# Optimization experiments

Measured on AMD Instinct MI355X. Metric: run time of the kernel, lower is better.

Reference implementation:

```python
import jax, jax.numpy as jnp
import numpy as np

N_ENVS, N_AGENTS, OBS_DIM, HIDDEN, HEAD = 4096, 64, 256, 512, 32


def setup_inputs() -> dict:
    key = jax.random.key(0)
    ks = jax.random.split(key, 10)
    s = 0.02
    return {
        "obs": jax.random.normal(ks[0], (N_ENVS, N_AGENTS, OBS_DIM), jnp.float32),
        # shared 2-layer MLP params (applied identically to every agent slice)
        "W1": jax.random.normal(ks[1], (OBS_DIM, HIDDEN), jnp.float32) * s,
        "b1": jnp.zeros((HIDDEN,), jnp.float32),
        "W2": jax.random.normal(ks[2], (HIDDEN, HIDDEN), jnp.float32) * s,
        "b2": jnp.zeros((HIDDEN,), jnp.float32),
        # per-agent head params, stacked over agent axis
        "HW1": jax.random.normal(ks[3], (N_AGENTS, HIDDEN, HEAD), jnp.float32) * s,
        "Hb1": jnp.zeros((N_AGENTS, HEAD), jnp.float32),
        "HW2": jax.random.normal(ks[4], (N_AGENTS, HEAD), jnp.float32) * s,
        "Hb2": jnp.zeros((N_AGENTS,), jnp.float32),
    }


def reference(obs, W1, b1, W2, b2, HW1, Hb1, HW2, Hb2):
    # shared MLP: same weights for every agent -> single batched GEMM over (env, agent)
    h = jax.nn.relu(jnp.einsum('ead,dh->eah', obs, W1) + b1)   # [E, A, H]
    feat = jax.nn.relu(jnp.einsum('eah,hk->eak', h, W2) + b2)  # [E, A, H]
    # per-agent heads: grouped GEMM via einsum over stacked weights
    g = jax.nn.relu(jnp.einsum('eah,ahk->eak', feat, HW1) + Hb1)  # [E, A, 32]
    actions = jax.nn.sigmoid(jnp.einsum('eak,ak->ea', g, HW2) + Hb2)  # [E, A]
    return actions
```

## Files before the change

kernel.cpp:

```cpp
#include <hip/hip_runtime.h>
#include <hip/hip_bf16.h>
#include <math.h>

#define N_ENVS   4096
#define N_AGENTS 64
#define OBS_DIM  256
#define HIDDEN   512
#define HEADK    32
#define BROWS    128

typedef __attribute__((ext_vector_type(8))) short bf16x8;
typedef __attribute__((ext_vector_type(4))) float f32x4;

static __device__ __forceinline__ unsigned cvt_pk_bf16(float lo, float hi) {
    unsigned r;
    asm("v_cvt_pk_bf16_f32 %0, %1, %2" : "=v"(r) : "v"(lo), "v"(hi));
    return r;
}

static __device__ __forceinline__ unsigned short f2bf(float x) {
    union { float f; unsigned int u; } v; v.f = x;
    unsigned int r = (v.u + 0x7FFFu + ((v.u >> 16) & 1u)) >> 16;
    return (unsigned short)r;
}

__global__ void prep_weights_kernel(const float* __restrict__ W1,
                                    const float* __restrict__ W2,
                                    const float* __restrict__ HW1,
                                    unsigned short* __restrict__ W1T,
                                    unsigned short* __restrict__ W2T,
                                    unsigned short* __restrict__ HW1T) {
    int id = blockIdx.x * 256 + threadIdx.x;
    if (id < 131072) {
        int k = id >> 9, n = id & 511;
        W1T[n * 256 + k] = f2bf(W1[id]);
    } else if (id < 131072 + 262144) {
        int t = id - 131072;
        int k = t >> 9, n = t & 511;
        W2T[n * 512 + k] = f2bf(W2[t]);
    } else if (id < 131072 + 262144 + 1048576) {
        int t = id - (131072 + 262144);
        int ag = t >> 14;
        int rem = t & 16383;
        int hh = rem >> 5, c = rem & 31;
        HW1T[((ag << 5) + c) * 512 + hh] = f2bf(HW1[t]);
    }
}

__launch_bounds__(512, 2)
__global__ void fused_mlp_kernel(const float* __restrict__ obs,
                                 const float* __restrict__ b1,
                                 const float* __restrict__ b2,
                                 const float* __restrict__ Hb1,
                                 const float* __restrict__ HW2,
                                 const float* __restrict__ Hb2,
                                 const unsigned short* __restrict__ W1T,
                                 const unsigned short* __restrict__ W2T,
                                 const unsigned short* __restrict__ HW1T,
                                 float* __restrict__ out) {
    __shared__ unsigned short buf[BROWS * 512];
    __shared__ float gpart[BROWS * 36];

    const int tid  = threadIdx.x;
    const int lane = tid & 63;
    const int wid  = tid >> 6;
    const int l15  = lane & 15;
    const int lk   = lane >> 4;
    const int e0   = blockIdx.x * 64;
    const int ap   = blockIdx.y;

    const f32x4 fzero = {0.f, 0.f, 0.f, 0.f};

    const unsigned short* bbase1 = W1T + (size_t)(wid * 64 + l15) * 256 + lk * 8;
    const unsigned short* bbase2 = W2T + (size_t)(wid * 64 + l15) * 512 + lk * 8;

    bf16x8 bcur[4];

    {
        const float* base = obs + (size_t)(((unsigned)e0 * 64u + 2u * (unsigned)ap) * 256u);
        float4 v[16];
        #pragma unroll
        for (int g = 0; g < 8; ++g) {
            unsigned gi  = (unsigned)tid + 512u * g;
            unsigned row = gi >> 5;
            unsigned kg  = (gi & 31u) << 3;
            unsigned fidx = (row & 63u) * 16384u + (row >> 6) * 256u + kg;
            v[2 * g]     = *reinterpret_cast<const float4*>(base + fidx);
            v[2 * g + 1] = *reinterpret_cast<const float4*>(base + fidx + 4);
        }
        #pragma unroll
        for (int ni = 0; ni < 4; ++ni)
            bcur[ni] = *reinterpret_cast<const bf16x8*>(bbase1 + ni * 16 * 256);
        #pragma unroll
        for (int g = 0; g < 8; ++g) {
            unsigned gi  = (unsigned)tid + 512u * g;
            unsigned row = gi >> 5;
            unsigned kg  = (gi & 31u) << 3;
            uint4 w;
            w.x = cvt_pk_bf16(v[2 * g].x, v[2 * g].y);
            w.y = cvt_pk_bf16(v[2 * g].z, v[2 * g].w);
            w.z = cvt_pk_bf16(v[2 * g + 1].x, v[2 * g + 1].y);
            w.w = cvt_pk_bf16(v[2 * g + 1].z, v[2 * g + 1].w);
            unsigned byt = (row * 512u + kg * 2u) ^ ((row & 7u) << 4);
            *reinterpret_cast<uint4*>(&buf[byt >> 1]) = w;
        }
    }
    __syncthreads();

    f32x4 acc[8][4];
    #pragma unroll
    for (int i = 0; i < 8; ++i)
        #pragma unroll
        for (int j = 0; j < 4; ++j) acc[i][j] = fzero;

    {
        #pragma unroll 1
        for (int ks = 0; ks < 8; ++ks) {
            bf16x8 bnxt[4];
            const int kn = (ks < 7 ? ks + 1 : 7);
            #pragma unroll
            for (int ni = 0; ni < 4; ++ni)
                bnxt[ni] = *reinterpret_cast<const bf16x8*>(bbase1 + ni * 16 * 256 + kn * 32);
            const int kk = ks * 32 + lk * 8;
            #pragma unroll
            for (int mi = 0; mi < 8; ++mi) {
                int row = mi * 16 + l15;
                bf16x8 af = *reinterpret_cast<const bf16x8*>(&buf[((row * 512 + kk * 2) ^ ((row & 7) << 4)) >> 1]);
                #pragma unroll
                for (int ni = 0; ni < 4; ++ni)
                    acc[mi][ni] = __builtin_amdgcn_mfma_f32_16x16x32_bf16(bcur[ni], af, acc[mi][ni], 0, 0, 0);
            }
            #pragma unroll
            for (int ni = 0; ni < 4; ++ni) bcur[ni] = bnxt[ni];
        }
    }

    bf16x8 bcur2[4];
    #pragma unroll
    for (int ni = 0; ni < 4; ++ni)
        bcur2[ni] = *reinterpret_cast<const bf16x8*>(bbase2 + ni * 16 * 512);

    __syncthreads();

    #pragma unroll
    for (int ni = 0; ni < 4; ++ni) {
        const int col0 = wid * 64 + ni * 16 + lk * 4;
        const float4 bias = *reinterpret_cast<const float4*>(b1 + col0);
        #pragma unroll
        for (int mi = 0; mi < 8; ++mi) {
            int row = mi * 16 + l15;
            float v0 = fmaxf(acc[mi][ni][0] + bias.x, 0.f);
            float v1 = fmaxf(acc[mi][ni][1] + bias.y, 0.f);
            float v2 = fmaxf(acc[mi][ni][2] + bias.z, 0.f);
            float v3 = fmaxf(acc[mi][ni][3] + bias.w, 0.f);
            uint2 w = { cvt_pk_bf16(v0, v1), cvt_pk_bf16(v2, v3) };
            int byt = (row * 1024 + col0 * 2) ^ ((row & 7) << 4);
            *reinterpret_cast<uint2*>(&buf[byt >> 1]) = w;
        }
    }
    __syncthreads();

    #pragma unroll
    for (int i = 0; i < 8; ++i)
        #pragma unroll
        for (int j = 0; j < 4; ++j) acc[i][j] = fzero;

    {
        #pragma unroll 1
        for (int ks = 0; ks < 16; ++ks) {
            bf16x8 bnxt[4];
            const int kn = (ks < 15 ? ks + 1 : 15);
            #pragma unroll
            for (int ni = 0; ni < 4; ++ni)
                bnxt[ni] = *reinterpret_cast<const bf16x8*>(bbase2 + ni * 16 * 512 + kn * 32);
            const int kk = ks * 32 + lk * 8;
            #pragma unroll
            for (int mi = 0; mi < 8; ++mi) {
                int row = mi * 16 + l15;
                bf16x8 af = *reinterpret_cast<const bf16x8*>(&buf[((row * 1024 + kk * 2) ^ ((row & 7) << 4)) >> 1]);
                #pragma unroll
                for (int ni = 0; ni < 4; ++ni)
                    acc[mi][ni] = __builtin_amdgcn_mfma_f32_16x16x32_bf16(bcur2[ni], af, acc[mi][ni], 0, 0, 0);
            }
            #pragma unroll
            for (int ni = 0; ni < 4; ++ni) bcur2[ni] = bnxt[ni];
        }
    }
    __syncthreads();

    #pragma unroll
    for (int ni = 0; ni < 4; ++ni) {
        const int col0 = wid * 64 + ni * 16 + lk * 4;
        const float4 bias = *reinterpret_cast<const float4*>(b2 + col0);
        #pragma unroll
        for (int mi = 0; mi < 8; ++mi) {
            int row = mi * 16 + l15;
            float v0 = fmaxf(acc[mi][ni][0] + bias.x, 0.f);
            float v1 = fmaxf(acc[mi][ni][1] + bias.y, 0.f);
            float v2 = fmaxf(acc[mi][ni][2] + bias.z, 0.f);
            float v3 = fmaxf(acc[mi][ni][3] + bias.w, 0.f);
            uint2 w = { cvt_pk_bf16(v0, v1), cvt_pk_bf16(v2, v3) };
            int byt = (row * 1024 + col0 * 2) ^ ((row & 7) << 4);
            *reinterpret_cast<uint2*>(&buf[byt >> 1]) = w;
        }
    }
    __syncthreads();

    {
        const int ja  = wid >> 2;
        const int hm  = wid & 3;
        const int a32 = ((2 * ap + ja) << 5);
        const unsigned short* hbase = HW1T + (size_t)(a32 + l15) * 512 + lk * 8;
        const int rowh = ja * 64 + hm * 16 + l15;
        f32x4 hacc[2] = {fzero, fzero};

        {
            bf16x8 hw0[8], hw1[8];
            #pragma unroll
            for (int ks = 0; ks < 8; ++ks) {
                hw0[ks] = *reinterpret_cast<const bf16x8*>(hbase + ks * 32);
                hw1[ks] = *reinterpret_cast<const bf16x8*>(hbase + 16 * 512 + ks * 32);
            }
            #pragma unroll
            for (int ks = 0; ks < 8; ++ks) {
                const int kk = ks * 32 + lk * 8;
                int byt = (rowh * 1024 + kk * 2) ^ ((rowh & 7) << 4);
                bf16x8 afh = *reinterpret_cast<const bf16x8*>(&buf[byt >> 1]);
                hacc[0] = __builtin_amdgcn_mfma_f32_16x16x32_bf16(hw0[ks], afh, hacc[0], 0, 0, 0);
                hacc[1] = __builtin_amdgcn_mfma_f32_16x16x32_bf16(hw1[ks], afh, hacc[1], 0, 0, 0);
            }
        }
        {
            bf16x8 hw0[8], hw1[8];
            #pragma unroll
            for (int ks = 0; ks < 8; ++ks) {
                hw0[ks] = *reinterpret_cast<const bf16x8*>(hbase + (ks + 8) * 32);
                hw1[ks] = *reinterpret_cast<const bf16x8*>(hbase + 16 * 512 + (ks + 8) * 32);
            }
            #pragma unroll
            for (int ks = 0; ks < 8; ++ks) {
                const int kk = (ks + 8) * 32 + lk * 8;
                int byt = (rowh * 1024 + kk * 2) ^ ((rowh & 7) << 4);
                bf16x8 afh = *reinterpret_cast<const bf16x8*>(&buf[byt >> 1]);
                hacc[0] = __builtin_amdgcn_mfma_f32_16x16x32_bf16(hw0[ks], afh, hacc[0], 0, 0, 0);
                hacc[1] = __builtin_amdgcn_mfma_f32_16x16x32_bf16(hw1[ks], afh, hacc[1], 0, 0, 0);
            }
        }

        #pragma unroll
        for (int ni = 0; ni < 2; ++ni) {
            const int col0 = ni * 16 + lk * 4;
            const float4 hbias = *reinterpret_cast<const float4*>(Hb1 + a32 + col0);
            float4 g;
            g.x = fmaxf(hacc[ni][0] + hbias.x, 0.f);
            g.y = fmaxf(hacc[ni][1] + hbias.y, 0.f);
            g.z = fmaxf(hacc[ni][2] + hbias.z, 0.f);
            g.w = fmaxf(hacc[ni][3] + hbias.w, 0.f);
            *reinterpret_cast<float4*>(&gpart[rowh * 36 + col0]) = g;
        }
    }
    __syncthreads();

    if (tid < BROWS) {
        int e = tid & 63, j = tid >> 6;
        int a = 2 * ap + j;
        float x = Hb2[a];
        #pragma unroll 2
        for (int k = 0; k < 32; ++k)
            x += gpart[tid * 36 + k] * HW2[(a << 5) + k];
        out[(size_t)(e0 + e) * N_AGENTS + a] = 1.f / (1.f + expf(-x));
    }
}

extern "C" void kernel_launch(void* const* d_in, const int* in_sizes, int n_in,
                              void* d_out, int out_size, void* d_ws, size_t ws_size,
                              hipStream_t stream) {
    const float* obs = (const float*)d_in[0];
    const float* W1  = (const float*)d_in[1];
    const float* b1  = (const float*)d_in[2];
    const float* W2  = (const float*)d_in[3];
    const float* b2  = (const float*)d_in[4];
    const float* HW1 = (const float*)d_in[5];
    const float* Hb1 = (const float*)d_in[6];
    const float* HW2 = (const float*)d_in[7];
    const float* Hb2 = (const float*)d_in[8];
    float* out = (float*)d_out;

    unsigned short* W1T  = (unsigned short*)d_ws;
    unsigned short* W2T  = W1T + 131072;
    unsigned short* HW1T = W2T + 262144;

    prep_weights_kernel<<<5632, 256, 0, stream>>>(W1, W2, HW1, W1T, W2T, HW1T);

    dim3 grid(N_ENVS / 64, N_AGENTS / 2);
    fused_mlp_kernel<<<grid, 512, 0, stream>>>(obs, b1, b2, Hb1, HW2, Hb2,
                                               W1T, W2T, HW1T, out);
}
```

Baseline: 325.9 us.

## Make fused MLP kernel persistent over eight env tiles with prefetched obs loads

The grid shrinks from 2048 blocks to 256 persistent blocks. Each block loops over 8 consecutive 64-env tiles for one agent pair. The obs loads for the next tile are issued before the head GEMM of the current tile, and are converted and stored to LDS after it, so global latency overlaps compute. The head weight loads become a software-pipelined loop instead of fully preloading 16 registers per half. The risk is fewer blocks than one per CU on a 256-CU device, with no block-level latency hiding, plus higher register pressure from holding the prefetched obs values.

```diff
diff --git a/kernel.cpp b/kernel.cpp
--- a/kernel.cpp
+++ b/kernel.cpp
@@ -66,31 +66,32 @@
     const int wid  = tid >> 6;
     const int l15  = lane & 15;
     const int lk   = lane >> 4;
-    const int e0   = blockIdx.x * 64;
-    const int ap   = blockIdx.y;
+    const int ap   = blockIdx.x & 31;
+    const int oct  = blockIdx.x >> 5;
 
     const f32x4 fzero = {0.f, 0.f, 0.f, 0.f};
 
     const unsigned short* bbase1 = W1T + (size_t)(wid * 64 + l15) * 256 + lk * 8;
     const unsigned short* bbase2 = W2T + (size_t)(wid * 64 + l15) * 512 + lk * 8;
 
-    bf16x8 bcur[4];
-
+    unsigned g_fidx[8];
+    #pragma unroll
+    for (int g = 0; g < 8; ++g) {
+        unsigned gi  = (unsigned)tid + 512u * g;
+        unsigned row = gi >> 5;
+        unsigned kg  = (gi & 31u) << 3;
+        g_fidx[g] = (row & 63u) * 16384u + (row >> 6) * 256u + kg;
+    }
+    const unsigned tile0_base = ((unsigned)(oct * 512) * 64u + 2u * (unsigned)ap) * 256u;
+
+    float4 v[16];
     {
-        const float* base = obs + (size_t)(((unsigned)e0 * 64u + 2u * (unsigned)ap) * 256u);
-        float4 v[16];
+        const float* base = obs + tile0_base;
         #pragma unroll
         for (int g = 0; g < 8; ++g) {
-            unsigned gi  = (unsigned)tid + 512u * g;
-            unsigned row = gi >> 5;
-            unsigned kg  = (gi & 31u) << 3;
-            unsigned fidx = (row & 63u) * 16384u + (row >> 6) * 256u + kg;
-            v[2 * g]     = *reinterpret_cast<const float4*>(base + fidx);
-            v[2 * g + 1] = *reinterpret_cast<const float4*>(base + fidx + 4);
-        }
-        #pragma unroll
-        for (int ni = 0; ni < 4; ++ni)
-            bcur[ni] = *reinterpret_cast<const bf16x8*>(bbase1 + ni * 16 * 256);
+            v[2 * g]     = *reinterpret_cast<const float4*>(base + g_fidx[g]);
+            v[2 * g + 1] = *reinterpret_cast<const float4*>(base + g_fidx[g] + 4);
+        }
         #pragma unroll
         for (int g = 0; g < 8; ++g) {
             unsigned gi  = (unsigned)tid + 512u * g;
@@ -105,170 +106,183 @@
             *reinterpret_cast<uint4*>(&buf[byt >> 1]) = w;
         }
     }
-    __syncthreads();
-
-    f32x4 acc[8][4];
-    #pragma unroll
-    for (int i = 0; i < 8; ++i)
-        #pragma unroll
-        for (int j = 0; j < 4; ++j) acc[i][j] = fzero;
-
-    {
-        #pragma unroll 1
-        for (int ks = 0; ks < 8; ++ks) {
-            bf16x8 bnxt[4];
-            const int kn = (ks < 7 ? ks + 1 : 7);
+
+    #pragma unroll 1
+    for (int t = 0; t < 8; ++t) {
+        __syncthreads();
+
+        f32x4 acc[8][4];
+        #pragma unroll
+        for (int i = 0; i < 8; ++i)
+            #pragma unroll
+            for (int j = 0; j < 4; ++j) acc[i][j] = fzero;
+
+        {
+            bf16x8 bcur[4];
             #pragma unroll
             for (int ni = 0; ni < 4; ++ni)
-                bnxt[ni] = *reinterpret_cast<const bf16x8*>(bbase1 + ni * 16 * 256 + kn * 32);
-            const int kk = ks * 32 + lk * 8;
+                bcur[ni] = *reinterpret_cast<const bf16x8*>(bbase1 + ni * 16 * 256);
+            #pragma unroll 1
+            for (int ks = 0; ks < 8; ++ks) {
+                bf16x8 bnxt[4];
+                const int kn = (ks < 7 ? ks + 1 : 7);
+                #pragma unroll
+                for (int ni = 0; ni < 4; ++ni)
+                    bnxt[ni] = *reinterpret_cast<const bf16x8*>(bbase1 + ni * 16 * 256 + kn * 32);
+                const int kk = ks * 32 + lk * 8;
+                #pragma unroll
+                for (int mi = 0; mi < 8; ++mi) {
+                    int row = mi * 16 + l15;
+                    bf16x8 af = *reinterpret_cast<const bf16x8*>(&buf[((row * 512 + kk * 2) ^ ((row & 7) << 4)) >> 1]);
+                    #pragma unroll
+                    for (int ni = 0; ni < 4; ++ni)
+                        acc[mi][ni] = __builtin_amdgcn_mfma_f32_16x16x32_bf16(bcur[ni], af, acc[mi][ni], 0, 0, 0);
+                }
+                #pragma unroll
+                for (int ni = 0; ni < 4; ++ni) bcur[ni] = bnxt[ni];
+            }
+        }
+
+        bf16x8 bcur2[4];
+        #pragma unroll
+        for (int ni = 0; ni < 4; ++ni)
+            bcur2[ni] = *reinterpret_cast<const bf16x8*>(bbase2 + ni * 16 * 512);
+
+        __syncthreads();
+
+        #pragma unroll
+        for (int ni = 0; ni < 4; ++ni) {
+            const int col0 = wid * 64 + ni * 16 + lk * 4;
+            const float4 bias = *reinterpret_cast<const float4*>(b1 + col0);
             #pragma unroll
             for (int mi = 0; mi < 8; ++mi) {
                 int row = mi * 16 + l15;
-                bf16x8 af = *reinterpret_cast<const bf16x8*>(&buf[((row * 512 + kk * 2) ^ ((row & 7) << 4)) >> 1]);
+                float v0 = fmaxf(acc[mi][ni][0] + bias.x, 0.f);
+                float v1 = fmaxf(acc[mi][ni][1] + bias.y, 0.f);
+                float v2 = fmaxf(acc[mi][ni][2] + bias.z, 0.f);
+                float v3 = fmaxf(acc[mi][ni][3] + bias.w, 0.f);
+                uint2 w = { cvt_pk_bf16(v0, v1), cvt_pk_bf16(v2, v3) };
+                int byt = (row * 1024 + col0 * 2) ^ ((row & 7) << 4);
+                *reinterpret_cast<uint2*>(&buf[byt >> 1]) = w;
+            }
+        }
+        __syncthreads();
+
+        #pragma unroll
+        for (int i = 0; i < 8; ++i)
+            #pragma unroll
+            for (int j = 0; j < 4; ++j) acc[i][j] = fzero;
+
+        {
+            #pragma unroll 1
+            for (int ks = 0; ks < 16; ++ks) {
+                bf16x8 bnxt[4];
+                const int kn = (ks < 15 ? ks + 1 : 15);
                 #pragma unroll
                 for (int ni = 0; ni < 4; ++ni)
-                    acc[mi][ni] = __builtin_amdgcn_mfma_f32_16x16x32_bf16(bcur[ni], af, acc[mi][ni], 0, 0, 0);
-            }
-            #pragma unroll
-            for (int ni = 0; ni < 4; ++ni) bcur[ni] = bnxt[ni];
-        }
-    }
-
-    bf16x8 bcur2[4];
-    #pragma unroll
-    for (int ni = 0; ni < 4; ++ni)
-        bcur2[ni] = *reinterpret_cast<const bf16x8*>(bbase2 + ni * 16 * 512);
-
-    __syncthreads();
-
-    #pragma unroll
-    for (int ni = 0; ni < 4; ++ni) {
-        const int col0 = wid * 64 + ni * 16 + lk * 4;
-        const float4 bias = *reinterpret_cast<const float4*>(b1 + col0);
-        #pragma unroll
-        for (int mi = 0; mi < 8; ++mi) {
-            int row = mi * 16 + l15;
-            float v0 = fmaxf(acc[mi][ni][0] + bias.x, 0.f);
-            float v1 = fmaxf(acc[mi][ni][1] + bias.y, 0.f);
-            float v2 = fmaxf(acc[mi][ni][2] + bias.z, 0.f);
-            float v3 = fmaxf(acc[mi][ni][3] + bias.w, 0.f);
-            uint2 w = { cvt_pk_bf16(v0, v1), cvt_pk_bf16(v2, v3) };
-            int byt = (row * 1024 + col0 * 2) ^ ((row & 7) << 4);
-            *reinterpret_cast<uint2*>(&buf[byt >> 1]) = w;
-        }
-    }
-    __syncthreads();
-
-    #pragma unroll
-    for (int i = 0; i < 8; ++i)
-        #pragma unroll
-        for (int j = 0; j < 4; ++j) acc[i][j] = fzero;
-
-    {
-        #pragma unroll 1
-        for (int ks = 0; ks < 16; ++ks) {
-            bf16x8 bnxt[4];
-            const int kn = (ks < 15 ? ks + 1 : 15);
-            #pragma unroll
-            for (int ni = 0; ni < 4; ++ni)
-                bnxt[ni] = *reinterpret_cast<const bf16x8*>(bbase2 + ni * 16 * 512 + kn * 32);
-            const int kk = ks * 32 + lk * 8;
+                    bnxt[ni] = *reinterpret_cast<const bf16x8*>(bbase2 + ni * 16 * 512 + kn * 32);
+                const int kk = ks * 32 + lk * 8;
+                #pragma unroll
+                for (int mi = 0; mi < 8; ++mi) {
+                    int row = mi * 16 + l15;
+                    bf16x8 af = *reinterpret_cast<const bf16x8*>(&buf[((row * 1024 + kk * 2) ^ ((row & 7) << 4)) >> 1]);
+                    #pragma unroll
+                    for (int ni = 0; ni < 4; ++ni)
+                        acc[mi][ni] = __builtin_amdgcn_mfma_f32_16x16x32_bf16(bcur2[ni], af, acc[mi][ni], 0, 0, 0);
+                }
+                #pragma unroll
+                for (int ni = 0; ni < 4; ++ni) bcur2[ni] = bnxt[ni];
+            }
+        }
+        __syncthreads();
+
+        #pragma unroll
+        for (int ni = 0; ni < 4; ++ni) {
+            const int col0 = wid * 64 + ni * 16 + lk * 4;
+            const float4 bias = *reinterpret_cast<const float4*>(b2 + col0);
             #pragma unroll
             for (int mi = 0; mi < 8; ++mi) {
                 int row = mi * 16 + l15;
-                bf16x8 af = *reinterpret_cast<const bf16x8*>(&buf[((row * 1024 + kk * 2) ^ ((row & 7) << 4)) >> 1]);
-                #pragma unroll
-                for (int ni = 0; ni < 4; ++ni)
-                    acc[mi][ni] = __builtin_amdgcn_mfma_f32_16x16x32_bf16(bcur2[ni], af, acc[mi][ni], 0, 0, 0);
-            }
-            #pragma unroll
-            for (int ni = 0; ni < 4; ++ni) bcur2[ni] = bnxt[ni];
-        }
-    }
-    __syncthreads();
-
-    #pragma unroll
-    for (int ni = 0; ni < 4; ++ni) {
-        const int col0 = wid * 64 + ni * 16 + lk * 4;
-        const float4 bias = *reinterpret_cast<const float4*>(b2 + col0);
-        #pragma unroll
-        for (int mi = 0; mi < 8; ++mi) {
-            int row = mi * 16 + l15;
-            float v0 = fmaxf(acc[mi][ni][0] + bias.x, 0.f);
-            float v1 = fmaxf(acc[mi][ni][1] + bias.y, 0.f);
-            float v2 = fmaxf(acc[mi][ni][2] + bias.z, 0.f);
-            float v3 = fmaxf(acc[mi][ni][3] + bias.w, 0.f);
-            uint2 w = { cvt_pk_bf16(v0, v1), cvt_pk_bf16(v2, v3) };
-            int byt = (row * 1024 + col0 * 2) ^ ((row & 7) << 4);
-            *reinterpret_cast<uint2*>(&buf[byt >> 1]) = w;
-        }
-    }
-    __syncthreads();
-
-    {
-        const int ja  = wid >> 2;
-        const int hm  = wid & 3;
-        const int a32 = ((2 * ap + ja) << 5);
-        const unsigned short* hbase = HW1T + (size_t)(a32 + l15) * 512 + lk * 8;
-        const int rowh = ja * 64 + hm * 16 + l15;
-        f32x4 hacc[2] = {fzero, fzero};
+                float v0 = fmaxf(acc[mi][ni][0] + bias.x, 0.f);
+                float v1 = fmaxf(acc[mi][ni][1] + bias.y, 0.f);
+                float v2 = fmaxf(acc[mi][ni][2] + bias.z, 0.f);
+                float v3 = fmaxf(acc[mi][ni][3] + bias.w, 0.f);
+                uint2 w = { cvt_pk_bf16(v0, v1), cvt_pk_bf16(v2, v3) };
+                int byt = (row * 1024 + col0 * 2) ^ ((row & 7) << 4);
+                *reinterpret_cast<uint2*>(&buf[byt >> 1]) = w;
+            }
+        }
+        __syncthreads();
 
         {
-            bf16x8 hw0[8], hw1[8];
-            #pragma unroll
-            for (int ks = 0; ks < 8; ++ks) {
-                hw0[ks] = *reinterpret_cast<const bf16x8*>(hbase + ks * 32);
-                hw1[ks] = *reinterpret_cast<const bf16x8*>(hbase + 16 * 512 + ks * 32);
-            }
-            #pragma unroll
-            for (int ks = 0; ks < 8; ++ks) {
+            if (t < 7) {
+                const float* base = obs + tile0_base + (unsigned)(t + 1) * 64u * 16384u;
+                #pragma unroll
+                for (int g = 0; g < 8; ++g) {
+                    v[2 * g]     = *reinterpret_cast<const float4*>(base + g_fidx[g]);
+                    v[2 * g + 1] = *reinterpret_cast<const float4*>(base + g_fidx[g] + 4);
+                }
+            }
+
+            const int ja  = wid >> 2;
+            const int hm  = wid & 3;
+            const int a32 = ((2 * ap + ja) << 5);
+            const unsigned short* hbase = HW1T + (size_t)(a32 + l15) * 512 + lk * 8;
+            const int rowh = ja * 64 + hm * 16 + l15;
+            f32x4 hacc[2] = {fzero, fzero};
+            bf16x8 hb0 = *reinterpret_cast<const bf16x8*>(hbase);
+            bf16x8 hb1 = *reinterpret_cast<const bf16x8*>(hbase + 16 * 512);
+            #pragma unroll 1
+            for (int ks = 0; ks < 16; ++ks) {
+                const int kn = (ks < 15 ? ks + 1 : 15);
+                bf16x8 hn0 = *reinterpret_cast<const bf16x8*>(hbase + kn * 32);
+                bf16x8 hn1 = *reinterpret_cast<const bf16x8*>(hbase + 16 * 512 + kn * 32);
                 const int kk = ks * 32 + lk * 8;
                 int byt = (rowh * 1024 + kk * 2) ^ ((rowh & 7) << 4);
                 bf16x8 afh = *reinterpret_cast<const bf16x8*>(&buf[byt >> 1]);
-                hacc[0] = __builtin_amdgcn_mfma_f32_16x16x32_bf16(hw0[ks], afh, hacc[0], 0, 0, 0);
-                hacc[1] = __builtin_amdgcn_mfma_f32_16x16x32_bf16(hw1[ks], afh, hacc[1], 0, 0, 0);
-            }
-        }
-        {
-            bf16x8 hw0[8], hw1[8];
-            #pragma unroll
-            for (int ks = 0; ks < 8; ++ks) {
-                hw0[ks] = *reinterpret_cast<const bf16x8*>(hbase + (ks + 8) * 32);
-                hw1[ks] = *reinterpret_cast<const bf16x8*>(hbase + 16 * 512 + (ks + 8) * 32);
-            }
-            #pragma unroll
-            for (int ks = 0; ks < 8; ++ks) {
-                const int kk = (ks + 8) * 32 + lk * 8;
-                int byt = (rowh * 1024 + kk * 2) ^ ((rowh & 7) << 4);
-                bf16x8 afh = *reinterpret_cast<const bf16x8*>(&buf[byt >> 1]);
-                hacc[0] = __builtin_amdgcn_mfma_f32_16x16x32_bf16(hw0[ks], afh, hacc[0], 0, 0, 0);
-                hacc[1] = __builtin_amdgcn_mfma_f32_16x16x32_bf16(hw1[ks], afh, hacc[1], 0, 0, 0);
-            }
-        }
-
-        #pragma unroll
-        for (int ni = 0; ni < 2; ++ni) {
-            const int col0 = ni * 16 + lk * 4;
-            const float4 hbias = *reinterpret_cast<const float4*>(Hb1 + a32 + col0);
-            float4 g;
-            g.x = fmaxf(hacc[ni][0] + hbias.x, 0.f);
-            g.y = fmaxf(hacc[ni][1] + hbias.y, 0.f);
-            g.z = fmaxf(hacc[ni][2] + hbias.z, 0.f);
-            g.w = fmaxf(hacc[ni][3] + hbias.w, 0.f);
-            *reinterpret_cast<float4*>(&gpart[rowh * 36 + col0]) = g;
-        }
-    }
-    __syncthreads();
-
-    if (tid < BROWS) {
-        int e = tid & 63, j = tid >> 6;
-        int a = 2 * ap + j;
-        float x = Hb2[a];
-        #pragma unroll 2
-        for (int k = 0; k < 32; ++k)
-            x += gpart[tid * 36 + k] * HW2[(a << 5) + k];
-        out[(size_t)(e0 + e) * N_AGENTS + a] = 1.f / (1.f + expf(-x));
+                hacc[0] = __builtin_amdgcn_mfma_f32_16x16x32_bf16(hb0, afh, hacc[0], 0, 0, 0);
+                hacc[1] = __builtin_amdgcn_mfma_f32_16x16x32_bf16(hb1, afh, hacc[1], 0, 0, 0);
+                hb0 = hn0; hb1 = hn1;
+            }
+            #pragma unroll
+            for (int ni = 0; ni < 2; ++ni) {
+                const int col0 = ni * 16 + lk * 4;
+                const float4 hbias = *reinterpret_cast<const float4*>(Hb1 + a32 + col0);
+                float4 g;
+                g.x = fmaxf(hacc[ni][0] + hbias.x, 0.f);
+                g.y = fmaxf(hacc[ni][1] + hbias.y, 0.f);
+                g.z = fmaxf(hacc[ni][2] + hbias.z, 0.f);
+                g.w = fmaxf(hacc[ni][3] + hbias.w, 0.f);
+                *reinterpret_cast<float4*>(&gpart[rowh * 36 + col0]) = g;
+            }
+        }
+        __syncthreads();
+
+        if (t < 7) {
+            #pragma unroll
+            for (int g = 0; g < 8; ++g) {
+                unsigned gi  = (unsigned)tid + 512u * g;
+                unsigned row = gi >> 5;
+                unsigned kg  = (gi & 31u) << 3;
+                uint4 w;
+                w.x = cvt_pk_bf16(v[2 * g].x, v[2 * g].y);
+                w.y = cvt_pk_bf16(v[2 * g].z, v[2 * g].w);
+                w.z = cvt_pk_bf16(v[2 * g + 1].x, v[2 * g + 1].y);
+                w.w = cvt_pk_bf16(v[2 * g + 1].z, v[2 * g + 1].w);
+                unsigned byt = (row * 512u + kg * 2u) ^ ((row & 7u) << 4);
+                *reinterpret_cast<uint4*>(&buf[byt >> 1]) = w;
+            }
+        }
+        if (tid < BROWS) {
+            int e = tid & 63, j = tid >> 6;
+            int a = 2 * ap + j;
+            int e0 = oct * 512 + t * 64;
+            float x = Hb2[a];
+            #pragma unroll 2
+            for (int k = 0; k < 32; ++k)
+                x += gpart[tid * 36 + k] * HW2[(a << 5) + k];
+            out[(size_t)(e0 + e) * N_AGENTS + a] = 1.f / (1.f + expf(-x));
+        }
     }
 }
 
@@ -292,7 +306,6 @@
 
     prep_weights_kernel<<<5632, 256, 0, stream>>>(W1, W2, HW1, W1T, W2T, HW1T);
 
-    dim3 grid(N_ENVS / 64, N_AGENTS / 2);
-    fused_mlp_kernel<<<grid, 512, 0, stream>>>(obs, b1, b2, Hb1, HW2, Hb2,
-                                               W1T, W2T, HW1T, out);
-}
+    fused_mlp_kernel<<<256, 512, 0, stream>>>(obs, b1, b2, Hb1, HW2, Hb2,
+                                              W1T, W2T, HW1T, out);
+}
```

Result: slower. 386.4 us (+18.6%).
